# Performance work log

Measured on AMD Instinct MI355X. Metric: run time of the kernel, lower is better.

Reference implementation:

```python
import jax, jax.numpy as jnp
import numpy as np

DIM, HEADS, DIM_HEAD = 512, 8, 64

def setup_inputs() -> dict:
    key = jax.random.key(0)
    ks = jax.random.split(key, 9)
    B, T = 4, 4096
    s = 1.0 / np.sqrt(DIM)
    x = jax.random.normal(ks[0], (B, T, DIM), dtype=jnp.float32)
    Wq = jax.random.uniform(ks[1], (DIM, DIM), jnp.float32, -s, s)
    Wk = jax.random.uniform(ks[2], (DIM, DIM), jnp.float32, -s, s)
    Wv = jax.random.uniform(ks[3], (DIM, DIM), jnp.float32, -s, s)
    Wp = jax.random.uniform(ks[4], (DIM, DIM), jnp.float32, -s, s)
    bq = jax.random.uniform(ks[5], (DIM,), jnp.float32, -s, s)
    bk = jax.random.uniform(ks[6], (DIM,), jnp.float32, -s, s)
    bv = jax.random.uniform(ks[7], (DIM,), jnp.float32, -s, s)
    bp = jax.random.uniform(ks[8], (DIM,), jnp.float32, -s, s)
    return {"x": x, "Wq": Wq, "bq": bq, "Wk": Wk, "bk": bk,
            "Wv": Wv, "bv": bv, "Wp": Wp, "bp": bp}

def reference(x, Wq, bq, Wk, bk, Wv, bv, Wp, bp):
    B, T, _ = x.shape
    H, D = HEADS, DIM_HEAD
    # projections -> [B, H, T, D]
    def proj(W, b):
        return (x @ W.T + b).reshape(B, T, H, D).transpose(0, 2, 1, 3)
    q = jax.nn.softmax(proj(Wq, bq), axis=-1)
    k = jax.nn.softmax(proj(Wk, bk), axis=-1)
    v = proj(Wv, bv)
    # l1 normalization: D_inv = 1 / <q, sum_t k>
    k_sum = k.sum(axis=2, keepdims=True)                 # [B,H,1,D]
    D_inv = 1.0 / (q * k_sum).sum(axis=-1, keepdims=True)  # [B,H,T,1]
    context = jnp.einsum('bhtd,bhte->bhde', k, v)        # small DxD per head
    out = jnp.einsum('bhtd,bhde->bhte', q, context) * D_inv + q
    out = out.transpose(0, 2, 1, 3).reshape(B, T, H * D)
    return out @ Wp.T + bp
```

## Files before the change

### kernel.cpp

```cpp
#include <hip/hip_runtime.h>

#define NTOK  16384
#define KDIM  512
#define NQKV  1536
#define TT    4096

using frag8   = __attribute__((ext_vector_type(8))) short;
using floatx4 = __attribute__((ext_vector_type(4))) float;

__device__ __forceinline__ unsigned short f2b(float f) {
  union { float f; unsigned u; } v; v.f = f;
  unsigned r = v.u + 0x7fffu + ((v.u >> 16) & 1u);
  return (unsigned short)(r >> 16);
}
__device__ __forceinline__ float b2f(unsigned short s) {
  union { unsigned u; float f; } v; v.u = ((unsigned)s) << 16; return v.f;
}
__device__ __forceinline__ float blo(unsigned w) {
  union { unsigned u; float f; } v; v.u = w << 16; return v.f;
}
__device__ __forceinline__ float bhi(unsigned w) {
  union { unsigned u; float f; } v; v.u = w & 0xffff0000u; return v.f;
}

__device__ __forceinline__ void gl_lds16(const void* g, void* l) {
  __builtin_amdgcn_global_load_lds((__attribute__((address_space(1))) const void*)g,
                                   (__attribute__((address_space(3))) void*)l,
                                   16, 0, 0);
}

__global__ __launch_bounds__(256) void cvt_all(
    const float* __restrict__ x,
    const float* __restrict__ Wq, const float* __restrict__ Wk,
    const float* __restrict__ Wv, const float* __restrict__ Wp,
    const float* __restrict__ bq, const float* __restrict__ bk,
    const float* __restrict__ bv,
    unsigned short* __restrict__ xb,
    unsigned short* __restrict__ wqkv, unsigned short* __restrict__ wp,
    float* __restrict__ bias_qkv) {
  const int blk = blockIdx.x;
  if (blk < 8192) {
    const size_t i = (size_t)blk * 256 + threadIdx.x;
    const float4 v = ((const float4*)x)[i];
    ushort4 o;
    o.x = f2b(v.x); o.y = f2b(v.y); o.z = f2b(v.z); o.w = f2b(v.w);
    ((ushort4*)xb)[i] = o;
    return;
  }
  int idx = (blk - 8192) * 256 + threadIdx.x;
  if (idx < 196608) {
    const int m = idx >> 7, c4 = (idx & 127) << 2;
    const float* W = (m < 512) ? Wq : ((m < 1024) ? Wk : Wv);
    const float4 v = *(const float4*)&W[(m & 511) * 512 + c4];
    ushort4 o;
    o.x = f2b(v.x); o.y = f2b(v.y); o.z = f2b(v.z); o.w = f2b(v.w);
    *(ushort4*)&wqkv[m * 512 + c4] = o;
    return;
  }
  idx -= 196608;
  if (idx < 65536) {
    const float4 v = ((const float4*)Wp)[idx];
    ushort4 o;
    o.x = f2b(v.x); o.y = f2b(v.y); o.z = f2b(v.z); o.w = f2b(v.w);
    ((ushort4*)wp)[idx] = o;
    return;
  }
  idx -= 65536;
  if (idx < 1536)
    bias_qkv[idx] = (idx < 512) ? bq[idx]
                  : ((idx < 1024) ? bk[idx - 512] : bv[idx - 1024]);
}

template<int SOFT>
__global__ __launch_bounds__(256, 2) void gemm_bt(
    const unsigned short* __restrict__ A,
    const unsigned short* __restrict__ Bm,
    const float* __restrict__ bias,
    void* __restrict__ C,
    int M, int N, int K, int ldc)
{
  __shared__ unsigned short sh[16640];
  unsigned short* As = sh;
  unsigned short* Bs = sh + 128 * 64;
  const int tid  = threadIdx.x;
  const int wave = tid >> 6;
  const int lane = tid & 63;
  const int quad = lane >> 4;
  const int lr   = lane & 15;
  const int sw7  = lr & 7;
  const int bid  = ((blockIdx.x & 7) * (gridDim.x >> 3)) + (blockIdx.x >> 3);
  const int nt   = N >> 7;
  const int bn   = (bid % nt) << 7;
  const int bm   = (bid / nt) << 7;
  const int half = wave >> 1;
  const int wm   = half << 6;
  const int wn   = (wave & 1) << 6;

  floatx4 acc[4][4] = {};

  const int srow = tid >> 3;
  const int scol = ((tid & 7) ^ ((tid >> 3) & 7)) << 3;
  const unsigned short* Ag = A + (size_t)(bm + srow) * K + scol;
  const unsigned short* Bg = Bm + (size_t)(bn + srow) * K + scol;
  unsigned short* Al = As + (wave << 9);
  unsigned short* Bl = Bs + (wave << 9);

  for (int k0 = 0; k0 < K; k0 += 64) {
    __syncthreads();
    gl_lds16(Ag + k0,                    Al);
    gl_lds16(Ag + (size_t)32 * K + k0,   Al + 2048);
    gl_lds16(Ag + (size_t)64 * K + k0,   Al + 4096);
    gl_lds16(Ag + (size_t)96 * K + k0,   Al + 6144);
    gl_lds16(Bg + k0,                    Bl);
    gl_lds16(Bg + (size_t)32 * K + k0,   Bl + 2048);
    gl_lds16(Bg + (size_t)64 * K + k0,   Bl + 4096);
    gl_lds16(Bg + (size_t)96 * K + k0,   Bl + 6144);
    __syncthreads();

#pragma unroll
    for (int kk = 0; kk < 2; kk++) {
      const int coff = ((((kk << 2) + quad) ^ sw7) << 3);
      frag8 af[4], bf[4];
#pragma unroll
      for (int i = 0; i < 4; i++)
        af[i] = *(const frag8*)&As[(wm + (i << 4) + lr) * 64 + coff];
#pragma unroll
      for (int j = 0; j < 4; j++)
        bf[j] = *(const frag8*)&Bs[(wn + (j << 4) + lr) * 64 + coff];
#pragma unroll
      for (int i = 0; i < 4; i++)
#pragma unroll
        for (int j = 0; j < 4; j++)
          acc[i][j] = __builtin_amdgcn_mfma_f32_16x16x32_bf16(af[i], bf[j], acc[i][j], 0, 0, 0);
    }
  }

  const int ccol0 = bn + wn + lr;

#pragma unroll
  for (int j = 0; j < 4; j++) {
    const float bv = bias[ccol0 + (j << 4)];
#pragma unroll
    for (int i = 0; i < 4; i++)
#pragma unroll
      for (int r = 0; r < 4; r++)
        acc[i][j][r] += bv;
  }

  if (SOFT) {
    const int region = (bn + wn) >> 9;
    if (region < 2) {
#pragma unroll
      for (int i = 0; i < 4; i++)
#pragma unroll
        for (int r = 0; r < 4; r++) {
          float e0 = __expf(acc[i][0][r]);
          float e1 = __expf(acc[i][1][r]);
          float e2 = __expf(acc[i][2][r]);
          float e3 = __expf(acc[i][3][r]);
          float s = e0 + e1 + e2 + e3;
          s += __shfl_xor(s, 1);
          s += __shfl_xor(s, 2);
          s += __shfl_xor(s, 4);
          s += __shfl_xor(s, 8);
          const float inv = 1.f / s;
          acc[i][0][r] = e0 * inv; acc[i][1][r] = e1 * inv;
          acc[i][2][r] = e2 * inv; acc[i][3][r] = e3 * inv;
        }
    }
    unsigned short* os = sh;
#pragma unroll
    for (int p = 0; p < 2; p++) {
      __syncthreads();
      if (half == p) {
#pragma unroll
        for (int i = 0; i < 4; i++)
#pragma unroll
          for (int j = 0; j < 4; j++)
#pragma unroll
            for (int r = 0; r < 4; r++)
              os[((i << 4) + (quad << 2) + r) * 132 + wn + (j << 4) + lr] = f2b(acc[i][j][r]);
      }
      __syncthreads();
#pragma unroll
      for (int it = 0; it < 4; it++) {
        const int idx = (it << 8) + tid;
        const int row = idx >> 4;
        const int c8  = (idx & 15) << 3;
        *(uint4*)((unsigned short*)C + (size_t)(bm + (p << 6) + row) * ldc + bn + c8) =
            *(const uint4*)&os[row * 132 + c8];
      }
    }
  } else {
    float* osf = (float*)sh;
#pragma unroll
    for (int p = 0; p < 2; p++) {
      __syncthreads();
      if (half == p) {
#pragma unroll
        for (int i = 0; i < 4; i++)
#pragma unroll
          for (int j = 0; j < 4; j++)
#pragma unroll
            for (int r = 0; r < 4; r++)
              osf[((i << 4) + (quad << 2) + r) * 130 + wn + (j << 4) + lr] = acc[i][j][r];
      }
      __syncthreads();
#pragma unroll
      for (int it = 0; it < 8; it++) {
        const int idx = (it << 8) + tid;
        const int row = idx >> 5;
        const int c4  = (idx & 31) << 2;
        *(float4*)((float*)C + (size_t)(bm + (p << 6) + row) * ldc + bn + c4) =
            *(const float4*)&osf[row * 130 + c4];
      }
    }
  }
}

__global__ __launch_bounds__(256) void kv_context(const unsigned short* __restrict__ qkv,
                                                  float* __restrict__ part,
                                                  float* __restrict__ ksp) {
  const int bid = blockIdx.x;
  const int tc  = bid & 31;
  const int bh  = bid >> 5;
  const int b   = bh >> 3, h = bh & 7;
  __shared__ float ks[16 * 64];
  __shared__ float vs[16 * 64];
  const int tid = threadIdx.x;
  const int ty = tid >> 4, tx = tid & 15;
  floatx4 acc[4] = {};
  floatx4 ksacc = {0.f, 0.f, 0.f, 0.f};

  const int si    = tid << 3;
  const int strow = si >> 7;
  const int sw    = si & 127;
  const int t0    = b * TT + tc * 128;
  const unsigned short* gcol = qkv + ((sw < 64) ? (512 + h * 64 + sw)
                                                : (1024 + h * 64 + (sw - 64)));
  float* sdst = (sw < 64) ? &ks[strow * 64 + sw] : &vs[strow * 64 + (sw - 64)];

  uint4 raw = *(const uint4*)(gcol + (size_t)(t0 + strow) * NQKV);
  for (int tt = 0; tt < 128; tt += 16) {
    __syncthreads();
    const floatx4 f0 = {blo(raw.x), bhi(raw.x), blo(raw.y), bhi(raw.y)};
    const floatx4 f1 = {blo(raw.z), bhi(raw.z), blo(raw.w), bhi(raw.w)};
    *(floatx4*)sdst = f0;
    *(floatx4*)(sdst + 4) = f1;
    __syncthreads();
    if (tt + 16 < 128)
      raw = *(const uint4*)(gcol + (size_t)(t0 + tt + 16 + strow) * NQKV);
#pragma unroll
    for (int t = 0; t < 16; t++) {
      const floatx4 vb = *(const floatx4*)&vs[t * 64 + (ty << 2)];
      const floatx4 kb = *(const floatx4*)&ks[t * 64 + (tx << 2)];
      acc[0] += vb.x * kb;
      acc[1] += vb.y * kb;
      acc[2] += vb.z * kb;
      acc[3] += vb.w * kb;
    }
    ksacc += *(const floatx4*)&ks[ty * 64 + (tx << 2)];
  }
  __syncthreads();
  *(floatx4*)&vs[ty * 64 + (tx << 2)] = ksacc;
  __syncthreads();

  float* pg = part + ((size_t)(tc * 32 + bh) << 12) + (size_t)(ty << 2) * 64 + (tx << 2);
#pragma unroll
  for (int i = 0; i < 4; i++)
    *(floatx4*)(pg + i * 64) = acc[i];

  if (tid < 64) {
    float s = 0.f;
    for (int t2 = 0; t2 < 16; t2++) s += vs[t2 * 64 + tid];
    ksp[(tc * 32 + bh) * 64 + tid] = s;
  }
}

__global__ __launch_bounds__(256) void ctx_reduce(const float* __restrict__ part,
                                                  const float* __restrict__ ksp,
                                                  unsigned short* __restrict__ ctxb) {
  const int bh = blockIdx.x / 5, g = blockIdx.x % 5;
  const int row = (g << 4) + (threadIdx.x >> 4);
  const int d0  = (threadIdx.x & 15) << 2;
  floatx4 s = {0.f, 0.f, 0.f, 0.f};
  if (row < 64) {
    const float* p = part + ((size_t)bh << 12) + row * 64 + d0;
    for (int c = 0; c < 32; c++)
      s += *(const floatx4*)(p + ((size_t)c << 17));
  } else if (row == 64) {
    const float* p = ksp + bh * 64 + d0;
    for (int c = 0; c < 32; c++)
      s += *(const floatx4*)(p + (c << 11));
  }
  ushort4 o;
  o.x = f2b(s.x); o.y = f2b(s.y); o.z = f2b(s.z); o.w = f2b(s.w);
  *(ushort4*)&ctxb[(size_t)bh * 5120 + (row << 6) + d0] = o;
}

__global__ __launch_bounds__(256) void attn_out(const unsigned short* __restrict__ qkv,
                                                const unsigned short* __restrict__ ctxb,
                                                unsigned short* __restrict__ opre) {
  const int tc = blockIdx.x >> 5;
  const int bh = blockIdx.x & 31;
  const int b = bh >> 3, h = bh & 7;
  const int t0 = b * TT + (tc << 6);
  __shared__ unsigned short sh[144 * 72];
  unsigned short* qs = sh;
  unsigned short* cs = sh + 64 * 72;
  unsigned short* os = cs;
  const int tid = threadIdx.x;

  for (int i = tid; i < 512; i += 256) {
    const int row = i >> 3, c8 = (i & 7) << 3;
    *(uint4*)&qs[row * 72 + c8] =
        *(const uint4*)&qkv[(size_t)(t0 + row) * NQKV + h * 64 + c8];
  }
  for (int i = tid; i < 640; i += 256) {
    const int row = i >> 3, c8 = (i & 7) << 3;
    *(uint4*)&cs[row * 72 + c8] =
        *(const uint4*)&ctxb[(size_t)bh * 5120 + (row << 6) + c8];
  }
  __syncthreads();

  const int lane = tid & 63, w = tid >> 6, quad = lane >> 4, lr = lane & 15;
  floatx4 acc[5] = {};
#pragma unroll
  for (int k2 = 0; k2 < 2; k2++) {
    const int d0 = (k2 << 5) + (quad << 3);
    const frag8 bf = *(const frag8*)&qs[((w << 4) + lr) * 72 + d0];
#pragma unroll
    for (int et = 0; et < 5; et++) {
      const frag8 af = *(const frag8*)&cs[(et * 16 + lr) * 72 + d0];
      acc[et] = __builtin_amdgcn_mfma_f32_16x16x32_bf16(af, bf, acc[et], 0, 0, 0);
    }
  }
  const float dinv = 1.f / __shfl(acc[4][0], lr);
  __syncthreads();

  const int trow = (w << 4) + lr;
#pragma unroll
  for (int et = 0; et < 4; et++)
#pragma unroll
    for (int r = 0; r < 4; r++) {
      const int e = et * 16 + (quad << 2) + r;
      const float qv = b2f(qs[trow * 72 + e]);
      os[trow * 72 + e] = f2b(acc[et][r] * dinv + qv);
    }
  __syncthreads();

  for (int i = tid; i < 512; i += 256) {
    const int row = i >> 3, c8 = (i & 7) << 3;
    *(uint4*)&opre[(size_t)(t0 + row) * KDIM + h * 64 + c8] = *(const uint4*)&os[row * 72 + c8];
  }
}

extern "C" void kernel_launch(void* const* d_in, const int* in_sizes, int n_in,
                              void* d_out, int out_size, void* d_ws, size_t ws_size,
                              hipStream_t stream) {
  (void)in_sizes; (void)n_in; (void)out_size; (void)ws_size;
  const float* x  = (const float*)d_in[0];
  const float* Wq = (const float*)d_in[1];
  const float* bq = (const float*)d_in[2];
  const float* Wk = (const float*)d_in[3];
  const float* bk = (const float*)d_in[4];
  const float* Wv = (const float*)d_in[5];
  const float* bv = (const float*)d_in[6];
  const float* Wp = (const float*)d_in[7];
  const float* bp = (const float*)d_in[8];

  char* w = (char*)d_ws;
  unsigned short* xb   = (unsigned short*)w; w += (size_t)NTOK * KDIM * 2;
  float* part          = (float*)xb;
  unsigned short* wqkv = (unsigned short*)w; w += (size_t)NQKV * KDIM * 2;
  unsigned short* wp   = (unsigned short*)w; w += (size_t)KDIM * KDIM * 2;
  float* bias_qkv      = (float*)w;          w += (size_t)NQKV * 4;
  float* ksp           = (float*)w;          w += (size_t)1024 * 64 * 4;
  unsigned short* ctxb = (unsigned short*)w; w += (size_t)32 * 80 * 64 * 2;
  unsigned short* qkv  = (unsigned short*)w; w += (size_t)NTOK * NQKV * 2;
  unsigned short* opre = (unsigned short*)w; w += (size_t)NTOK * KDIM * 2;

  cvt_all<<<9222, 256, 0, stream>>>(x, Wq, Wk, Wv, Wp, bq, bk, bv,
                                    xb, wqkv, wp, bias_qkv);
  gemm_bt<1><<<(NTOK / 128) * (NQKV / 128), 256, 0, stream>>>(
      xb, wqkv, bias_qkv, qkv, NTOK, NQKV, KDIM, NQKV);
  kv_context<<<1024, 256, 0, stream>>>(qkv, part, ksp);
  ctx_reduce<<<160, 256, 0, stream>>>(part, ksp, ctxb);
  attn_out<<<2048, 256, 0, stream>>>(qkv, ctxb, opre);
  gemm_bt<0><<<(NTOK / 128) * (KDIM / 128), 256, 0, stream>>>(
      opre, wp, bp, d_out, NTOK, KDIM, KDIM, KDIM);
}
```

Measured before the change: 178.3 us.

## Rewrite kv_context with async global-to-LDS double buffering and 8x8 register tiles

The kv_context kernel now has each 64-lane wave handle its own 128-token chunk. K/V tiles are fetched straight into LDS as bf16 with double buffering and explicit vmcnt waits, and the block-wide __syncthreads barriers are gone. Each lane accumulates an 8x8 outer-product tile in registers, which raises arithmetic intensity per LDS read and removes the fp32 conversion staging. The chunk indexing still produces 32 partials per head, so ctx_reduce is unchanged. The large accumulator array raises register pressure, and the fine-grained waitcnt control relies on gl_lds16 issuing exactly one vm op per call.

```diff
diff --git a/kernel.cpp b/kernel.cpp
--- a/kernel.cpp
+++ b/kernel.cpp
@@ -218,62 +218,82 @@
   }
 }
 
-__global__ __launch_bounds__(256) void kv_context(const unsigned short* __restrict__ qkv,
+__global__ __launch_bounds__(128) void kv_context(const unsigned short* __restrict__ qkv,
                                                   float* __restrict__ part,
                                                   float* __restrict__ ksp) {
   const int bid = blockIdx.x;
-  const int tc  = bid & 31;
-  const int bh  = bid >> 5;
+  const int tc  = bid & 15;
+  const int bh  = bid >> 4;
   const int b   = bh >> 3, h = bh & 7;
-  __shared__ float ks[16 * 64];
-  __shared__ float vs[16 * 64];
-  const int tid = threadIdx.x;
-  const int ty = tid >> 4, tx = tid & 15;
-  floatx4 acc[4] = {};
-  floatx4 ksacc = {0.f, 0.f, 0.f, 0.f};
-
-  const int si    = tid << 3;
-  const int strow = si >> 7;
-  const int sw    = si & 127;
-  const int t0    = b * TT + tc * 128;
-  const unsigned short* gcol = qkv + ((sw < 64) ? (512 + h * 64 + sw)
-                                                : (1024 + h * 64 + (sw - 64)));
-  float* sdst = (sw < 64) ? &ks[strow * 64 + sw] : &vs[strow * 64 + (sw - 64)];
-
-  uint4 raw = *(const uint4*)(gcol + (size_t)(t0 + strow) * NQKV);
-  for (int tt = 0; tt < 128; tt += 16) {
-    __syncthreads();
-    const floatx4 f0 = {blo(raw.x), bhi(raw.x), blo(raw.y), bhi(raw.y)};
-    const floatx4 f1 = {blo(raw.z), bhi(raw.z), blo(raw.w), bhi(raw.w)};
-    *(floatx4*)sdst = f0;
-    *(floatx4*)(sdst + 4) = f1;
-    __syncthreads();
-    if (tt + 16 < 128)
-      raw = *(const uint4*)(gcol + (size_t)(t0 + tt + 16 + strow) * NQKV);
-#pragma unroll
-    for (int t = 0; t < 16; t++) {
-      const floatx4 vb = *(const floatx4*)&vs[t * 64 + (ty << 2)];
-      const floatx4 kb = *(const floatx4*)&ks[t * 64 + (tx << 2)];
-      acc[0] += vb.x * kb;
-      acc[1] += vb.y * kb;
-      acc[2] += vb.z * kb;
-      acc[3] += vb.w * kb;
-    }
-    ksacc += *(const floatx4*)&ks[ty * 64 + (tx << 2)];
-  }
-  __syncthreads();
-  *(floatx4*)&vs[ty * 64 + (tx << 2)] = ksacc;
-  __syncthreads();
-
-  float* pg = part + ((size_t)(tc * 32 + bh) << 12) + (size_t)(ty << 2) * 64 + (tx << 2);
-#pragma unroll
-  for (int i = 0; i < 4; i++)
-    *(floatx4*)(pg + i * 64) = acc[i];
-
-  if (tid < 64) {
-    float s = 0.f;
-    for (int t2 = 0; t2 < 16; t2++) s += vs[t2 * 64 + tid];
-    ksp[(tc * 32 + bh) * 64 + tid] = s;
+  __shared__ __align__(16) unsigned short kvl[8192];
+  const int tid  = threadIdx.x;
+  const int w    = tid >> 6;
+  const int lane = tid & 63;
+  const int ey   = lane >> 3;
+  const int dx   = lane & 7;
+  const int t0   = b * TT + tc * 256 + w * 128;
+  const int chunk = tc * 2 + w;
+
+  unsigned short* const L = kvl + (w << 12);
+
+  const unsigned short* kg = qkv + (size_t)(t0 + ey) * NQKV + 512 + h * 64 + (dx << 3);
+  const unsigned short* vg = kg + 512;
+
+  auto ISSUE = [&](int s) {
+    unsigned short* B = L + ((s & 1) << 11);
+    const size_t roff = (size_t)(s << 4) * NQKV;
+    gl_lds16(kg + roff,                    B);
+    gl_lds16(kg + roff + (size_t)8 * NQKV, B + 512);
+    gl_lds16(vg + roff,                    B + 1024);
+    gl_lds16(vg + roff + (size_t)8 * NQKV, B + 1536);
+  };
+
+  float acc[8][8] = {};
+  float ksacc[8] = {};
+
+  ISSUE(0); ISSUE(1);
+#pragma unroll
+  for (int s = 0; s < 8; ++s) {
+    if (s < 7) { asm volatile("s_waitcnt vmcnt(4)" ::: "memory"); }
+    else       { asm volatile("s_waitcnt vmcnt(0)" ::: "memory"); }
+    __builtin_amdgcn_sched_barrier(0);
+    const unsigned short* ks = L + ((s & 1) << 11);
+    const unsigned short* vs = ks + 1024;
+#pragma unroll
+    for (int t = 0; t < 16; ++t) {
+      const uint4 kr = *(const uint4*)&ks[t * 64 + (dx << 3)];
+      const uint4 vr = *(const uint4*)&vs[t * 64 + (ey << 3)];
+      float kf[8] = {blo(kr.x), bhi(kr.x), blo(kr.y), bhi(kr.y),
+                     blo(kr.z), bhi(kr.z), blo(kr.w), bhi(kr.w)};
+      float vf[8] = {blo(vr.x), bhi(vr.x), blo(vr.y), bhi(vr.y),
+                     blo(vr.z), bhi(vr.z), blo(vr.w), bhi(vr.w)};
+#pragma unroll
+      for (int i = 0; i < 8; ++i) ksacc[i] += kf[i];
+#pragma unroll
+      for (int e = 0; e < 8; ++e)
+#pragma unroll
+        for (int d = 0; d < 8; ++d)
+          acc[e][d] += vf[e] * kf[d];
+    }
+    if (s + 2 < 8) {
+      asm volatile("s_waitcnt lgkmcnt(0)" ::: "memory");
+      __builtin_amdgcn_sched_barrier(0);
+      ISSUE(s + 2);
+    }
+  }
+
+  float* pg = part + ((size_t)(chunk * 32 + bh) << 12) + (size_t)(ey << 3) * 64 + (dx << 3);
+#pragma unroll
+  for (int e = 0; e < 8; ++e) {
+    floatx4 lo = {acc[e][0], acc[e][1], acc[e][2], acc[e][3]};
+    floatx4 hi = {acc[e][4], acc[e][5], acc[e][6], acc[e][7]};
+    *(floatx4*)(pg + e * 64)     = lo;
+    *(floatx4*)(pg + e * 64 + 4) = hi;
+  }
+  if (ey == 0) {
+#pragma unroll
+    for (int i = 0; i < 8; ++i)
+      ksp[(chunk * 32 + bh) * 64 + (dx << 3) + i] = ksacc[i];
   }
 }
 
@@ -384,7 +404,7 @@
                                     xb, wqkv, wp, bias_qkv);
   gemm_bt<1><<<(NTOK / 128) * (NQKV / 128), 256, 0, stream>>>(
       xb, wqkv, bias_qkv, qkv, NTOK, NQKV, KDIM, NQKV);
-  kv_context<<<1024, 256, 0, stream>>>(qkv, part, ksp);
+  kv_context<<<512, 128, 0, stream>>>(qkv, part, ksp);
   ctx_reduce<<<160, 256, 0, stream>>>(part, ksp, ctxb);
   attn_out<<<2048, 256, 0, stream>>>(qkv, ctxb, opre);
   gemm_bt<0><<<(NTOK / 128) * (KDIM / 128), 256, 0, stream>>>(
```

Result: slower. 373.0 us (+109.3%).

## Write K/V transposed from QKV GEMM epilogue and use MFMA for KV context

Applied to the files above, without the earlier changes.

The QKV GEMM epilogue now writes Q row-major into a compact buffer, and writes K and V transposed per (batch, head) as [d][t] through an LDS transpose. kv_context loads these transposed tiles with direct global-to-LDS copies and computes the V^T·K context with bf16 MFMA instead of scalar fp32 FMAs. The k-sum is taken from the LDS tile. ctx_reduce writes the context transposed to match the new orientation. This replaces a strided, scalar context kernel with a tensor-core one. In exchange the GEMM epilogue does strided transposed stores, and the region test now branches per block instead of per wave.

```diff
diff --git a/kernel.cpp b/kernel.cpp
--- a/kernel.cpp
+++ b/kernel.cpp
@@ -27,6 +27,9 @@
   __builtin_amdgcn_global_load_lds((__attribute__((address_space(1))) const void*)g,
                                    (__attribute__((address_space(3))) void*)l,
                                    16, 0, 0);
+}
+__device__ __forceinline__ floatx4 mfma16(frag8 a, frag8 b, floatx4 c) {
+  return __builtin_amdgcn_mfma_f32_16x16x32_bf16(a, b, c, 0, 0, 0);
 }
 
 __global__ __launch_bounds__(256) void cvt_all(
@@ -77,6 +80,8 @@
     const unsigned short* __restrict__ Bm,
     const float* __restrict__ bias,
     void* __restrict__ C,
+    unsigned short* __restrict__ kt,
+    unsigned short* __restrict__ vt,
     int M, int N, int K, int ldc)
 {
   __shared__ unsigned short sh[16640];
@@ -131,7 +136,7 @@
       for (int i = 0; i < 4; i++)
 #pragma unroll
         for (int j = 0; j < 4; j++)
-          acc[i][j] = __builtin_amdgcn_mfma_f32_16x16x32_bf16(af[i], bf[j], acc[i][j], 0, 0, 0);
+          acc[i][j] = mfma16(af[i], bf[j], acc[i][j]);
     }
   }
 
@@ -148,7 +153,7 @@
   }
 
   if (SOFT) {
-    const int region = (bn + wn) >> 9;
+    const int region = bn >> 9;
     if (region < 2) {
 #pragma unroll
       for (int i = 0; i < 4; i++)
@@ -168,27 +173,58 @@
           acc[i][2][r] = e2 * inv; acc[i][3][r] = e3 * inv;
         }
     }
-    unsigned short* os = sh;
-#pragma unroll
-    for (int p = 0; p < 2; p++) {
-      __syncthreads();
-      if (half == p) {
-#pragma unroll
-        for (int i = 0; i < 4; i++)
-#pragma unroll
-          for (int j = 0; j < 4; j++)
-#pragma unroll
-            for (int r = 0; r < 4; r++)
-              os[((i << 4) + (quad << 2) + r) * 132 + wn + (j << 4) + lr] = f2b(acc[i][j][r]);
+    if (region == 0) {
+      unsigned short* os = sh;
+#pragma unroll
+      for (int p = 0; p < 2; p++) {
+        __syncthreads();
+        if (half == p) {
+#pragma unroll
+          for (int i = 0; i < 4; i++)
+#pragma unroll
+            for (int j = 0; j < 4; j++)
+#pragma unroll
+              for (int r = 0; r < 4; r++)
+                os[((i << 4) + (quad << 2) + r) * 132 + wn + (j << 4) + lr] = f2b(acc[i][j][r]);
+        }
+        __syncthreads();
+#pragma unroll
+        for (int it = 0; it < 4; it++) {
+          const int idx = (it << 8) + tid;
+          const int row = idx >> 4;
+          const int c8  = (idx & 15) << 3;
+          *(uint4*)((unsigned short*)C + (size_t)(bm + (p << 6) + row) * ldc + bn + c8) =
+              *(const uint4*)&os[row * 132 + c8];
+        }
       }
-      __syncthreads();
-#pragma unroll
-      for (int it = 0; it < 4; it++) {
-        const int idx = (it << 8) + tid;
-        const int row = idx >> 4;
-        const int c8  = (idx & 15) << 3;
-        *(uint4*)((unsigned short*)C + (size_t)(bm + (p << 6) + row) * ldc + bn + c8) =
-            *(const uint4*)&os[row * 132 + c8];
+    } else {
+      unsigned short* T = (region == 1) ? kt : vt;
+      const int b   = bm >> 12;
+      const int tIn = bm & 4095;
+      unsigned short* osT = sh;
+#pragma unroll
+      for (int p = 0; p < 2; p++) {
+        __syncthreads();
+        if ((wave & 1) == p) {
+#pragma unroll
+          for (int i = 0; i < 4; i++)
+#pragma unroll
+            for (int j = 0; j < 4; j++)
+#pragma unroll
+              for (int r = 0; r < 4; r++)
+                osT[((j << 4) + lr) * 130 + wm + (i << 4) + (quad << 2) + r] =
+                    f2b(acc[i][j][r]);
+        }
+        __syncthreads();
+        const int hh = ((bn >> 6) + p) & 7;
+        unsigned short* Tb = T + (((size_t)(b << 3) + hh) << 18) + tIn;
+#pragma unroll
+        for (int it = 0; it < 4; it++) {
+          const int idx = (it << 8) + tid;
+          const int col = idx >> 4;
+          const int tg  = (idx & 15) << 3;
+          *(uint4*)&Tb[((size_t)col << 12) + tg] = *(const uint4*)&osT[col * 130 + tg];
+        }
       }
     }
   } else {
@@ -218,63 +254,70 @@
   }
 }
 
-__global__ __launch_bounds__(256) void kv_context(const unsigned short* __restrict__ qkv,
+__global__ __launch_bounds__(256) void kv_context(const unsigned short* __restrict__ kt,
+                                                  const unsigned short* __restrict__ vt,
                                                   float* __restrict__ part,
                                                   float* __restrict__ ksp) {
   const int bid = blockIdx.x;
   const int tc  = bid & 31;
   const int bh  = bid >> 5;
-  const int b   = bh >> 3, h = bh & 7;
-  __shared__ float ks[16 * 64];
-  __shared__ float vs[16 * 64];
-  const int tid = threadIdx.x;
-  const int ty = tid >> 4, tx = tid & 15;
+  __shared__ unsigned short sh[16384];
+  unsigned short* vsl = sh;
+  unsigned short* ksl = sh + 8192;
+  const int tid  = threadIdx.x;
+  const int wave = tid >> 6;
+  const int lane = tid & 63;
+  const int quad = lane >> 4;
+  const int lr   = lane & 15;
+  const int t0   = tc << 7;
+
+  const int lrow = lane >> 4;
+  const int lchk = lane & 15;
+  const unsigned short* vg = vt + ((size_t)bh << 18) + t0;
+  const unsigned short* kg = kt + ((size_t)bh << 18) + t0;
+#pragma unroll
+  for (int i = 0; i < 4; i++) {
+    const int rb  = (wave << 4) + (i << 2);
+    const int row = rb + lrow;
+    const int sc  = (lchk ^ (row & 7)) << 3;
+    gl_lds16(vg + ((size_t)row << 12) + sc, vsl + (rb << 7));
+    gl_lds16(kg + ((size_t)row << 12) + sc, ksl + (rb << 7));
+  }
+  __syncthreads();
+
   floatx4 acc[4] = {};
-  floatx4 ksacc = {0.f, 0.f, 0.f, 0.f};
-
-  const int si    = tid << 3;
-  const int strow = si >> 7;
-  const int sw    = si & 127;
-  const int t0    = b * TT + tc * 128;
-  const unsigned short* gcol = qkv + ((sw < 64) ? (512 + h * 64 + sw)
-                                                : (1024 + h * 64 + (sw - 64)));
-  float* sdst = (sw < 64) ? &ks[strow * 64 + sw] : &vs[strow * 64 + (sw - 64)];
-
-  uint4 raw = *(const uint4*)(gcol + (size_t)(t0 + strow) * NQKV);
-  for (int tt = 0; tt < 128; tt += 16) {
-    __syncthreads();
-    const floatx4 f0 = {blo(raw.x), bhi(raw.x), blo(raw.y), bhi(raw.y)};
-    const floatx4 f1 = {blo(raw.z), bhi(raw.z), blo(raw.w), bhi(raw.w)};
-    *(floatx4*)sdst = f0;
-    *(floatx4*)(sdst + 4) = f1;
-    __syncthreads();
-    if (tt + 16 < 128)
-      raw = *(const uint4*)(gcol + (size_t)(t0 + tt + 16 + strow) * NQKV);
-#pragma unroll
-    for (int t = 0; t < 16; t++) {
-      const floatx4 vb = *(const floatx4*)&vs[t * 64 + (ty << 2)];
-      const floatx4 kb = *(const floatx4*)&ks[t * 64 + (tx << 2)];
-      acc[0] += vb.x * kb;
-      acc[1] += vb.y * kb;
-      acc[2] += vb.z * kb;
-      acc[3] += vb.w * kb;
-    }
-    ksacc += *(const floatx4*)&ks[ty * 64 + (tx << 2)];
-  }
-  __syncthreads();
-  *(floatx4*)&vs[ty * 64 + (tx << 2)] = ksacc;
-  __syncthreads();
-
-  float* pg = part + ((size_t)(tc * 32 + bh) << 12) + (size_t)(ty << 2) * 64 + (tx << 2);
-#pragma unroll
-  for (int i = 0; i < 4; i++)
-    *(floatx4*)(pg + i * 64) = acc[i];
-
-  if (tid < 64) {
-    float s = 0.f;
-    for (int t2 = 0; t2 < 16; t2++) s += vs[t2 * 64 + tid];
-    ksp[(tc * 32 + bh) * 64 + tid] = s;
-  }
+  const int we = wave << 4;
+#pragma unroll
+  for (int ks = 0; ks < 4; ks++) {
+    const int co = ((((ks << 2) + quad) ^ (lr & 7)) << 3);
+    const frag8 af = *(const frag8*)&vsl[(we + lr) * 128 + co];
+    frag8 bfr[4];
+#pragma unroll
+    for (int j = 0; j < 4; j++)
+      bfr[j] = *(const frag8*)&ksl[((j << 4) + lr) * 128 + co];
+#pragma unroll
+    for (int j = 0; j < 4; j++)
+      acc[j] = mfma16(af, bfr[j], acc[j]);
+  }
+
+  float* pg = part + ((size_t)(tc * 32 + bh) << 12) + we + (quad << 2);
+#pragma unroll
+  for (int j = 0; j < 4; j++)
+    *(floatx4*)&pg[((j << 4) + lr) << 6] = acc[j];
+
+  const int r2 = tid >> 2;
+  const int q4 = tid & 3;
+  float s = 0.f;
+#pragma unroll
+  for (int c = 0; c < 4; c++) {
+    const int ch = ((q4 << 2) + c) ^ (r2 & 7);
+    const uint4 raw = *(const uint4*)&ksl[r2 * 128 + (ch << 3)];
+    s += blo(raw.x) + bhi(raw.x) + blo(raw.y) + bhi(raw.y)
+       + blo(raw.z) + bhi(raw.z) + blo(raw.w) + bhi(raw.w);
+  }
+  s += __shfl_xor(s, 1);
+  s += __shfl_xor(s, 2);
+  if (q4 == 0) ksp[(tc * 32 + bh) * 64 + r2] = s;
 }
 
 __global__ __launch_bounds__(256) void ctx_reduce(const float* __restrict__ part,
@@ -285,20 +328,25 @@
   const int d0  = (threadIdx.x & 15) << 2;
   floatx4 s = {0.f, 0.f, 0.f, 0.f};
   if (row < 64) {
-    const float* p = part + ((size_t)bh << 12) + row * 64 + d0;
+    const float* p = part + ((size_t)bh << 12) + (row << 6) + d0;
     for (int c = 0; c < 32; c++)
       s += *(const floatx4*)(p + ((size_t)c << 17));
-  } else if (row == 64) {
-    const float* p = ksp + bh * 64 + d0;
-    for (int c = 0; c < 32; c++)
-      s += *(const floatx4*)(p + (c << 11));
-  }
-  ushort4 o;
-  o.x = f2b(s.x); o.y = f2b(s.y); o.z = f2b(s.z); o.w = f2b(s.w);
-  *(ushort4*)&ctxb[(size_t)bh * 5120 + (row << 6) + d0] = o;
-}
-
-__global__ __launch_bounds__(256) void attn_out(const unsigned short* __restrict__ qkv,
+#pragma unroll
+    for (int i = 0; i < 4; i++)
+      ctxb[(size_t)bh * 5120 + ((size_t)(d0 + i) << 6) + row] = f2b(s[i]);
+  } else {
+    if (row == 64) {
+      const float* p = ksp + bh * 64 + d0;
+      for (int c = 0; c < 32; c++)
+        s += *(const floatx4*)(p + (c << 11));
+    }
+    ushort4 o;
+    o.x = f2b(s.x); o.y = f2b(s.y); o.z = f2b(s.z); o.w = f2b(s.w);
+    *(ushort4*)&ctxb[(size_t)bh * 5120 + (row << 6) + d0] = o;
+  }
+}
+
+__global__ __launch_bounds__(256) void attn_out(const unsigned short* __restrict__ qb,
                                                 const unsigned short* __restrict__ ctxb,
                                                 unsigned short* __restrict__ opre) {
   const int tc = blockIdx.x >> 5;
@@ -314,7 +362,7 @@
   for (int i = tid; i < 512; i += 256) {
     const int row = i >> 3, c8 = (i & 7) << 3;
     *(uint4*)&qs[row * 72 + c8] =
-        *(const uint4*)&qkv[(size_t)(t0 + row) * NQKV + h * 64 + c8];
+        *(const uint4*)&qb[(size_t)(t0 + row) * KDIM + h * 64 + c8];
   }
   for (int i = tid; i < 640; i += 256) {
     const int row = i >> 3, c8 = (i & 7) << 3;
@@ -332,7 +380,7 @@
 #pragma unroll
     for (int et = 0; et < 5; et++) {
       const frag8 af = *(const frag8*)&cs[(et * 16 + lr) * 72 + d0];
-      acc[et] = __builtin_amdgcn_mfma_f32_16x16x32_bf16(af, bf, acc[et], 0, 0, 0);
+      acc[et] = mfma16(af, bf, acc[et]);
     }
   }
   const float dinv = 1.f / __shfl(acc[4][0], lr);
@@ -380,13 +428,17 @@
   unsigned short* qkv  = (unsigned short*)w; w += (size_t)NTOK * NQKV * 2;
   unsigned short* opre = (unsigned short*)w; w += (size_t)NTOK * KDIM * 2;
 
+  unsigned short* qb  = qkv;
+  unsigned short* ktb = qkv + (size_t)NTOK * 512;
+  unsigned short* vtb = ktb + (size_t)32 * 64 * TT;
+
   cvt_all<<<9222, 256, 0, stream>>>(x, Wq, Wk, Wv, Wp, bq, bk, bv,
                                     xb, wqkv, wp, bias_qkv);
   gemm_bt<1><<<(NTOK / 128) * (NQKV / 128), 256, 0, stream>>>(
-      xb, wqkv, bias_qkv, qkv, NTOK, NQKV, KDIM, NQKV);
-  kv_context<<<1024, 256, 0, stream>>>(qkv, part, ksp);
+      xb, wqkv, bias_qkv, qb, ktb, vtb, NTOK, NQKV, KDIM, 512);
+  kv_context<<<1024, 256, 0, stream>>>(ktb, vtb, part, ksp);
   ctx_reduce<<<160, 256, 0, stream>>>(part, ksp, ctxb);
-  attn_out<<<2048, 256, 0, stream>>>(qkv, ctxb, opre);
+  attn_out<<<2048, 256, 0, stream>>>(qb, ctxb, opre);
   gemm_bt<0><<<(NTOK / 128) * (KDIM / 128), 256, 0, stream>>>(
-      opre, wp, bp, d_out, NTOK, KDIM, KDIM, KDIM);
-}
+      opre, wp, bp, d_out, nullptr, nullptr, NTOK, KDIM, KDIM, KDIM);
+}
```

Measured after the change: 174.6 us. 2.0% less time.
